# Optimization experiments

Measured on AMD Instinct MI355X. Metric: run time of the kernel, lower is better.

## Reference

```python
import jax, jax.numpy as jnp
import numpy as np

NUM_TASKS = 1024
N_FEATURES = 256
HIDDEN = 64
BATCH = 8192


def setup_inputs() -> dict:
    key = jax.random.key(0)
    k1, k2, k3, k4, k5 = jax.random.split(key, 5)
    x = jax.random.normal(k1, (BATCH, N_FEATURES), dtype=jnp.float32)
    task_ids = jax.random.randint(k2, (BATCH,), 0, NUM_TASKS, dtype=jnp.int32)
    # embedding tables, stored flat like nn.Embedding.weight
    l1_emb = jax.random.normal(k3, (NUM_TASKS, HIDDEN * N_FEATURES), dtype=jnp.float32) * 0.02
    l2_emb = jax.random.normal(k4, (NUM_TASKS, HIDDEN * HIDDEN), dtype=jnp.float32) * 0.02
    l3_emb = jax.random.normal(k5, (NUM_TASKS, HIDDEN), dtype=jnp.float32) * 0.02
    return {"x": x, "task_ids": task_ids, "l1_emb": l1_emb, "l2_emb": l2_emb, "l3_emb": l3_emb}


def reference(x, task_ids, l1_emb, l2_emb, l3_emb):
    # gather per-sample weight matrices (torch: emb.weight[task_ids].view(...))
    l1 = l1_emb[task_ids].reshape(-1, N_FEATURES, HIDDEN)   # [B, F, H]
    l2 = l2_emb[task_ids].reshape(-1, HIDDEN, HIDDEN)        # [B, H, H]
    l3 = l3_emb[task_ids]                                    # [B, H]
    gelu = lambda v: jax.nn.gelu(v, approximate=False)       # torch nn.GELU default = exact erf
    h1 = gelu(jnp.einsum('bf,bfh->bh', x, l1))               # [B, H]
    h2 = gelu(jnp.einsum('bh,bhk->bk', h1, l2))              # [B, H]
    out = jnp.einsum('bh,bh->b', h2, l3)[:, None]            # [B, 1] (matches squeeze(-1) of [B,1,1])
    return jax.nn.sigmoid(out)
```

## Files before the change

kernel.cpp:

```cpp
#include <hip/hip_runtime.h>
#include <math.h>

#define BATCH 8192
#define NTASK 1024
#define NF 256
#define NH 64
#define MAXBLK 2816


__global__ __launch_bounds__(1024) void prep_kernel(const int* __restrict__ task_ids,
                                                    int* __restrict__ order,
                                                    int* __restrict__ desc,
                                                    int* __restrict__ nblk) {
    __shared__ int cnt[NTASK];
    __shared__ int wsum[16];
    const int tid  = threadIdx.x;
    const int lane = tid & 63;
    const int wv   = tid >> 6;

    cnt[tid] = 0;
    __syncthreads();

    int myids[8];
    #pragma unroll
    for (int k = 0; k < 8; ++k) myids[k] = task_ids[tid + k * 1024];
    #pragma unroll
    for (int k = 0; k < 8; ++k) atomicAdd(&cnt[myids[k]], 1);
    __syncthreads();

    const int c  = cnt[tid];
    const int nb = (c + 3) >> 2;
    const int packed = (c << 12) | nb;

    int v = packed;
    #pragma unroll
    for (int d = 1; d < 64; d <<= 1) {
        int u = __shfl_up(v, d);
        if (lane >= d) v += u;
    }
    if (lane == 63) wsum[wv] = v;
    __syncthreads();
    if (wv == 0 && lane < 16) {
        int s = wsum[lane];
        #pragma unroll
        for (int d = 1; d < 16; d <<= 1) {
            int u = __shfl_up(s, d);
            if (lane >= d) s += u;
        }
        wsum[lane] = s;
    }
    __syncthreads();

    const int incl = ((wv > 0) ? wsum[wv - 1] : 0) + v;
    const int excl = incl - packed;
    const int offC   = excl >> 12;
    const int bstart = excl & 0xFFF;
    if (tid == NTASK - 1) nblk[0] = incl & 0xFFF;
    cnt[tid] = offC;
    __syncthreads();

    #pragma unroll
    for (int k = 0; k < 8; ++k) {
        int i = tid + k * 1024;
        int pos = atomicAdd(&cnt[myids[k]], 1);
        order[pos] = i;
    }
    for (int k = 0; k < nb; ++k) {
        int S = min(4, c - 4 * k);
        desc[bstart + k] = (tid << 15) | ((offC + 4 * k) << 2) | (S - 1);
    }
}

__device__ __forceinline__ float gelu_exact(float s) {
    return 0.5f * s * (1.f + erff(s * 0.70710678118654752440f));
}
__device__ __forceinline__ float4 gelu4(float4 v) {
    return make_float4(gelu_exact(v.x), gelu_exact(v.y), gelu_exact(v.z), gelu_exact(v.w));
}
__device__ __forceinline__ float4 fma4(float s, float4 w, float4 a) {
    a.x = fmaf(s, w.x, a.x); a.y = fmaf(s, w.y, a.y);
    a.z = fmaf(s, w.z, a.z); a.w = fmaf(s, w.w, a.w);
    return a;
}
__device__ __forceinline__ float4 xor_reduce4(float4 v, int m) {
    v.x += __shfl_xor(v.x, m); v.y += __shfl_xor(v.y, m);
    v.z += __shfl_xor(v.z, m); v.w += __shfl_xor(v.w, m);
    return v;
}

__global__ __launch_bounds__(256) void mlp_quad(
    const float* __restrict__ x,
    const int*   __restrict__ order,
    const int*   __restrict__ desc,
    const int*   __restrict__ nblk,
    const float* __restrict__ l1_emb,
    const float* __restrict__ l2_emb,
    const float* __restrict__ l3_emb,
    float*       __restrict__ out)
{
    const int nb = nblk[0];
    const int P  = blockIdx.x;
    if (P >= nb) return;
    const int qc = nb >> 3, r = nb & 7;
    const int xcd = P & 7, j = P >> 3;
    const int b = (xcd < r ? xcd * (qc + 1) : r * (qc + 1) + (xcd - r) * qc) + j;

    const int d  = desc[b];
    const int S  = (d & 3) + 1;
    const int st = (d >> 2) & 8191;
    const int t  = d >> 15;

    const int tid  = threadIdx.x;
    const int lane = tid & 63;
    const int w    = tid >> 6;
    const int cq   = lane & 15;
    const int grp  = lane >> 4;

    __shared__ float  xs[4][NF];
    __shared__ float4 red[4][4][16];

    const int myi = order[st + min(w, S - 1)];

    {
        const float4* x4 = (const float4*)x;
        ((float4*)xs)[w * 64 + lane] = x4[(size_t)myi * 64 + lane];
    }
    __syncthreads();

    const float4* W1 = (const float4*)(l1_emb + (size_t)t * (NF * NH));
    float4 a0 = make_float4(0.f,0.f,0.f,0.f), a1 = a0, a2 = a0, a3 = a0;
    const int fbase = w * 64 + grp * 16;
    #pragma unroll
    for (int jj = 0; jj < 16; ++jj) {
        const int f = fbase + jj;
        float4 wv = W1[f * 16 + cq];
        a0 = fma4(xs[0][f], wv, a0);
        a1 = fma4(xs[1][f], wv, a1);
        a2 = fma4(xs[2][f], wv, a2);
        a3 = fma4(xs[3][f], wv, a3);
    }
    a0 = xor_reduce4(xor_reduce4(a0, 16), 32);
    a1 = xor_reduce4(xor_reduce4(a1, 16), 32);
    a2 = xor_reduce4(xor_reduce4(a2, 16), 32);
    a3 = xor_reduce4(xor_reduce4(a3, 16), 32);
    if (lane < 16) {
        red[w][0][lane] = a0; red[w][1][lane] = a1;
        red[w][2][lane] = a2; red[w][3][lane] = a3;
    }
    __syncthreads();

    float4 A = red[0][w][grp], B = red[1][w][grp];
    float4 C = red[2][w][grp], D = red[3][w][grp];
    const float4 hv = gelu4(make_float4(A.x+B.x+C.x+D.x, A.y+B.y+C.y+D.y,
                                        A.z+B.z+C.z+D.z, A.w+B.w+C.w+D.w));

    const float4* W2 = (const float4*)(l2_emb + (size_t)t * (NH * NH));
    float4 acc = make_float4(0.f,0.f,0.f,0.f);
    acc = fma4(hv.x, W2[(grp * 4 + 0) * 16 + cq], acc);
    acc = fma4(hv.y, W2[(grp * 4 + 1) * 16 + cq], acc);
    acc = fma4(hv.z, W2[(grp * 4 + 2) * 16 + cq], acc);
    acc = fma4(hv.w, W2[(grp * 4 + 3) * 16 + cq], acc);
    acc = xor_reduce4(xor_reduce4(acc, 16), 32);
    float4 g = gelu4(acc);

    const float4* L3 = (const float4*)(l3_emb + (size_t)t * NH);
    float4 w3 = L3[cq];
    float dot = g.x * w3.x + g.y * w3.y + g.z * w3.z + g.w * w3.w;
    #pragma unroll
    for (int m = 1; m < 16; m <<= 1) dot += __shfl_xor(dot, m);
    if (lane == 0 && w < S)
        out[myi] = 1.f / (1.f + expf(-dot));
}

extern "C" void kernel_launch(void* const* d_in, const int* in_sizes, int n_in,
                              void* d_out, int out_size, void* d_ws, size_t ws_size,
                              hipStream_t stream) {
    const float* x        = (const float*)d_in[0];
    const int*   task_ids = (const int*)  d_in[1];
    const float* l1_emb   = (const float*)d_in[2];
    const float* l2_emb   = (const float*)d_in[3];
    const float* l3_emb   = (const float*)d_in[4];
    float*       out      = (float*)d_out;

    int* ws    = (int*)d_ws;
    int* order = ws;
    int* desc  = ws + BATCH;
    int* nblk  = ws + BATCH + MAXBLK;

    prep_kernel<<<1, 1024, 0, stream>>>(task_ids, order, desc, nblk);
    mlp_quad   <<<MAXBLK, 256, 0, stream>>>(x, order, desc, nblk,
                                            l1_emb, l2_emb, l3_emb, out);
}
```

Measured before the change: 28.70 us.

## Group up to eight same-task samples per block to reuse gathered weights

Samples sharing a task are now packed into blocks of up to eight instead of four, so each block's read of a task's 64 KB layer-1 weight matrix serves twice as many samples. The goal is to cut the number of blocks and the repeated weight traffic, which dominates this memory-bound kernel. The layer-2 and layer-3 weight loads are also hoisted ahead of the first barrier so they overlap the x load. In exchange each thread carries eight float4 accumulators, raising register pressure, and tasks with few samples leave more of each block idle.

```diff
diff --git a/kernel.cpp b/kernel.cpp
--- a/kernel.cpp
+++ b/kernel.cpp
@@ -5,7 +5,7 @@
 #define NTASK 1024
 #define NF 256
 #define NH 64
-#define MAXBLK 2816
+#define MAXBLK 1920
 
 
 __global__ __launch_bounds__(1024) void prep_kernel(const int* __restrict__ task_ids,
@@ -29,7 +29,7 @@
     __syncthreads();
 
     const int c  = cnt[tid];
-    const int nb = (c + 3) >> 2;
+    const int nb = (c + 7) >> 3;
     const int packed = (c << 12) | nb;
 
     int v = packed;
@@ -66,8 +66,8 @@
         order[pos] = i;
     }
     for (int k = 0; k < nb; ++k) {
-        int S = min(4, c - 4 * k);
-        desc[bstart + k] = (tid << 15) | ((offC + 4 * k) << 2) | (S - 1);
+        int S = min(8, c - 8 * k);
+        desc[bstart + k] = (tid << 16) | ((offC + 8 * k) << 3) | (S - 1);
     }
 }
 
@@ -87,8 +87,11 @@
     v.z += __shfl_xor(v.z, m); v.w += __shfl_xor(v.w, m);
     return v;
 }
-
-__global__ __launch_bounds__(256) void mlp_quad(
+__device__ __forceinline__ float4 add4(float4 a, float4 b) {
+    return make_float4(a.x + b.x, a.y + b.y, a.z + b.z, a.w + b.w);
+}
+
+__global__ __launch_bounds__(256) void mlp_oct(
     const float* __restrict__ x,
     const int*   __restrict__ order,
     const int*   __restrict__ desc,
@@ -106,9 +109,9 @@
     const int b = (xcd < r ? xcd * (qc + 1) : r * (qc + 1) + (xcd - r) * qc) + j;
 
     const int d  = desc[b];
-    const int S  = (d & 3) + 1;
-    const int st = (d >> 2) & 8191;
-    const int t  = d >> 15;
+    const int S  = (d & 7) + 1;
+    const int st = (d >> 3) & 8191;
+    const int t  = d >> 16;
 
     const int tid  = threadIdx.x;
     const int lane = tid & 63;
@@ -116,60 +119,79 @@
     const int cq   = lane & 15;
     const int grp  = lane >> 4;
 
-    __shared__ float  xs[4][NF];
-    __shared__ float4 red[4][4][16];
-
-    const int myi = order[st + min(w, S - 1)];
+    __shared__ float  xs[8][NF];
+    __shared__ float4 red[4][8][16];
+
+    const int iA = order[st + min(w,     S - 1)];
+    const int iB = order[st + min(w + 4, S - 1)];
+    const int i0 = order[st + min(2 * w,     S - 1)];
+    const int i1 = order[st + min(2 * w + 1, S - 1)];
 
     {
         const float4* x4 = (const float4*)x;
-        ((float4*)xs)[w * 64 + lane] = x4[(size_t)myi * 64 + lane];
-    }
+        ((float4*)xs)[w * 64 + lane]         = x4[(size_t)iA * 64 + lane];
+        ((float4*)xs)[(w + 4) * 64 + lane]   = x4[(size_t)iB * 64 + lane];
+    }
+
+    const float4* W2 = (const float4*)(l2_emb + (size_t)t * (NH * NH));
+    const float4* L3 = (const float4*)(l3_emb + (size_t)t * NH);
+    const float4 w2q0 = W2[(grp * 4 + 0) * 16 + cq];
+    const float4 w2q1 = W2[(grp * 4 + 1) * 16 + cq];
+    const float4 w2q2 = W2[(grp * 4 + 2) * 16 + cq];
+    const float4 w2q3 = W2[(grp * 4 + 3) * 16 + cq];
+    const float4 w3   = L3[cq];
+
     __syncthreads();
 
     const float4* W1 = (const float4*)(l1_emb + (size_t)t * (NF * NH));
-    float4 a0 = make_float4(0.f,0.f,0.f,0.f), a1 = a0, a2 = a0, a3 = a0;
+    float4 acc[8];
+    #pragma unroll
+    for (int s = 0; s < 8; ++s) acc[s] = make_float4(0.f, 0.f, 0.f, 0.f);
     const int fbase = w * 64 + grp * 16;
     #pragma unroll
     for (int jj = 0; jj < 16; ++jj) {
         const int f = fbase + jj;
         float4 wv = W1[f * 16 + cq];
-        a0 = fma4(xs[0][f], wv, a0);
-        a1 = fma4(xs[1][f], wv, a1);
-        a2 = fma4(xs[2][f], wv, a2);
-        a3 = fma4(xs[3][f], wv, a3);
-    }
-    a0 = xor_reduce4(xor_reduce4(a0, 16), 32);
-    a1 = xor_reduce4(xor_reduce4(a1, 16), 32);
-    a2 = xor_reduce4(xor_reduce4(a2, 16), 32);
-    a3 = xor_reduce4(xor_reduce4(a3, 16), 32);
+        #pragma unroll
+        for (int s = 0; s < 8; ++s)
+            acc[s] = fma4(xs[s][f], wv, acc[s]);
+    }
+    #pragma unroll
+    for (int s = 0; s < 8; ++s)
+        acc[s] = xor_reduce4(xor_reduce4(acc[s], 16), 32);
     if (lane < 16) {
-        red[w][0][lane] = a0; red[w][1][lane] = a1;
-        red[w][2][lane] = a2; red[w][3][lane] = a3;
-    }
-    __syncthreads();
-
-    float4 A = red[0][w][grp], B = red[1][w][grp];
-    float4 C = red[2][w][grp], D = red[3][w][grp];
-    const float4 hv = gelu4(make_float4(A.x+B.x+C.x+D.x, A.y+B.y+C.y+D.y,
-                                        A.z+B.z+C.z+D.z, A.w+B.w+C.w+D.w));
-
-    const float4* W2 = (const float4*)(l2_emb + (size_t)t * (NH * NH));
-    float4 acc = make_float4(0.f,0.f,0.f,0.f);
-    acc = fma4(hv.x, W2[(grp * 4 + 0) * 16 + cq], acc);
-    acc = fma4(hv.y, W2[(grp * 4 + 1) * 16 + cq], acc);
-    acc = fma4(hv.z, W2[(grp * 4 + 2) * 16 + cq], acc);
-    acc = fma4(hv.w, W2[(grp * 4 + 3) * 16 + cq], acc);
-    acc = xor_reduce4(xor_reduce4(acc, 16), 32);
-    float4 g = gelu4(acc);
-
-    const float4* L3 = (const float4*)(l3_emb + (size_t)t * NH);
-    float4 w3 = L3[cq];
-    float dot = g.x * w3.x + g.y * w3.y + g.z * w3.z + g.w * w3.w;
-    #pragma unroll
-    for (int m = 1; m < 16; m <<= 1) dot += __shfl_xor(dot, m);
-    if (lane == 0 && w < S)
-        out[myi] = 1.f / (1.f + expf(-dot));
+        #pragma unroll
+        for (int s = 0; s < 8; ++s) red[w][s][lane] = acc[s];
+    }
+    __syncthreads();
+
+    const float4 hv0 = gelu4(add4(add4(red[0][2*w][grp],   red[1][2*w][grp]),
+                                  add4(red[2][2*w][grp],   red[3][2*w][grp])));
+    const float4 hv1 = gelu4(add4(add4(red[0][2*w+1][grp], red[1][2*w+1][grp]),
+                                  add4(red[2][2*w+1][grp], red[3][2*w+1][grp])));
+
+    float4 b0 = make_float4(0.f, 0.f, 0.f, 0.f);
+    float4 b1 = make_float4(0.f, 0.f, 0.f, 0.f);
+    b0 = fma4(hv0.x, w2q0, b0);  b1 = fma4(hv1.x, w2q0, b1);
+    b0 = fma4(hv0.y, w2q1, b0);  b1 = fma4(hv1.y, w2q1, b1);
+    b0 = fma4(hv0.z, w2q2, b0);  b1 = fma4(hv1.z, w2q2, b1);
+    b0 = fma4(hv0.w, w2q3, b0);  b1 = fma4(hv1.w, w2q3, b1);
+    b0 = xor_reduce4(xor_reduce4(b0, 16), 32);
+    b1 = xor_reduce4(xor_reduce4(b1, 16), 32);
+    float4 g0 = gelu4(b0);
+    float4 g1 = gelu4(b1);
+
+    float d0 = g0.x * w3.x + g0.y * w3.y + g0.z * w3.z + g0.w * w3.w;
+    float d1 = g1.x * w3.x + g1.y * w3.y + g1.z * w3.z + g1.w * w3.w;
+    #pragma unroll
+    for (int m = 1; m < 16; m <<= 1) {
+        d0 += __shfl_xor(d0, m);
+        d1 += __shfl_xor(d1, m);
+    }
+    if (lane == 0) {
+        if (2 * w < S)     out[i0] = 1.f / (1.f + expf(-d0));
+        if (2 * w + 1 < S) out[i1] = 1.f / (1.f + expf(-d1));
+    }
 }
 
 extern "C" void kernel_launch(void* const* d_in, const int* in_sizes, int n_in,
@@ -188,6 +210,6 @@
     int* nblk  = ws + BATCH + MAXBLK;
 
     prep_kernel<<<1, 1024, 0, stream>>>(task_ids, order, desc, nblk);
-    mlp_quad   <<<MAXBLK, 256, 0, stream>>>(x, order, desc, nblk,
+    mlp_oct    <<<MAXBLK, 256, 0, stream>>>(x, order, desc, nblk,
                                             l1_emb, l2_emb, l3_emb, out);
 }
```

Measured after the change: 30.47 us. 6.2% more time.

## Give each wave its own sample for layer 1, dropping the cross-wave LDS reduction

Applied to the files above, without the earlier changes.

Layer 1 is repartitioned so that each wave computes the full 256-feature dot product for one sample, instead of all four waves splitting features across the four samples. This removes the shared reduction buffer and the second block barrier, and the hidden vector is redistributed within the wave by shuffles. The cost is that every wave now reads the whole task W1 matrix, so per-block global/L2 reads of W1 go up fourfold instead of being shared across samples.

```diff
diff --git a/kernel.cpp b/kernel.cpp
--- a/kernel.cpp
+++ b/kernel.cpp
@@ -87,6 +87,10 @@
     v.z += __shfl_xor(v.z, m); v.w += __shfl_xor(v.w, m);
     return v;
 }
+__device__ __forceinline__ float4 shfl4(float4 v, int src) {
+    return make_float4(__shfl(v.x, src), __shfl(v.y, src),
+                       __shfl(v.z, src), __shfl(v.w, src));
+}
 
 __global__ __launch_bounds__(256) void mlp_quad(
     const float* __restrict__ x,
@@ -116,8 +120,7 @@
     const int cq   = lane & 15;
     const int grp  = lane >> 4;
 
-    __shared__ float  xs[4][NF];
-    __shared__ float4 red[4][4][16];
+    __shared__ float xs[4][NF];
 
     const int myi = order[st + min(w, S - 1)];
 
@@ -128,34 +131,24 @@
     __syncthreads();
 
     const float4* W1 = (const float4*)(l1_emb + (size_t)t * (NF * NH));
-    float4 a0 = make_float4(0.f,0.f,0.f,0.f), a1 = a0, a2 = a0, a3 = a0;
-    const int fbase = w * 64 + grp * 16;
-    #pragma unroll
-    for (int jj = 0; jj < 16; ++jj) {
-        const int f = fbase + jj;
-        float4 wv = W1[f * 16 + cq];
-        a0 = fma4(xs[0][f], wv, a0);
-        a1 = fma4(xs[1][f], wv, a1);
-        a2 = fma4(xs[2][f], wv, a2);
-        a3 = fma4(xs[3][f], wv, a3);
+    const float4* xsw = ((const float4*)xs) + w * 64;
+    float4 a = make_float4(0.f, 0.f, 0.f, 0.f);
+    #pragma unroll 4
+    for (int q = 0; q < 16; ++q) {
+        const float4 xq = xsw[grp * 16 + q];
+        const int f = grp * 64 + q * 4;
+        a = fma4(xq.x, W1[(f + 0) * 16 + cq], a);
+        a = fma4(xq.y, W1[(f + 1) * 16 + cq], a);
+        a = fma4(xq.z, W1[(f + 2) * 16 + cq], a);
+        a = fma4(xq.w, W1[(f + 3) * 16 + cq], a);
     }
-    a0 = xor_reduce4(xor_reduce4(a0, 16), 32);
-    a1 = xor_reduce4(xor_reduce4(a1, 16), 32);
-    a2 = xor_reduce4(xor_reduce4(a2, 16), 32);
-    a3 = xor_reduce4(xor_reduce4(a3, 16), 32);
-    if (lane < 16) {
-        red[w][0][lane] = a0; red[w][1][lane] = a1;
-        red[w][2][lane] = a2; red[w][3][lane] = a3;
-    }
-    __syncthreads();
+    a = xor_reduce4(xor_reduce4(a, 16), 32);
+    const float4 h1q = gelu4(a);
 
-    float4 A = red[0][w][grp], B = red[1][w][grp];
-    float4 C = red[2][w][grp], D = red[3][w][grp];
-    const float4 hv = gelu4(make_float4(A.x+B.x+C.x+D.x, A.y+B.y+C.y+D.y,
-                                        A.z+B.z+C.z+D.z, A.w+B.w+C.w+D.w));
+    const float4 hv = shfl4(h1q, grp * 17);
 
     const float4* W2 = (const float4*)(l2_emb + (size_t)t * (NH * NH));
-    float4 acc = make_float4(0.f,0.f,0.f,0.f);
+    float4 acc = make_float4(0.f, 0.f, 0.f, 0.f);
     acc = fma4(hv.x, W2[(grp * 4 + 0) * 16 + cq], acc);
     acc = fma4(hv.y, W2[(grp * 4 + 1) * 16 + cq], acc);
     acc = fma4(hv.z, W2[(grp * 4 + 2) * 16 + cq], acc);
```

Result: slower. 38.64 us (median of 2 runs) (+34.6%).
